# Kernel tuning notes

Measured on AMD Instinct MI355X. Metric: run time of the kernel, lower is better.

Reference implementation:

```python
import jax, jax.numpy as jnp
import numpy as np

B, S = 256, 64
D_SLOT, D_TEXT, H, E = 256, 768, 512, 512
VOCAB = 1000
D_IN = D_SLOT + D_TEXT


def setup_inputs() -> dict:
    key = jax.random.key(0)
    ks = jax.random.split(key, 12)
    w = 0.05  # small init so GRU gates are not saturated
    return {
        "slot_ids": jax.random.randint(ks[0], (B, S), 0, VOCAB),
        "value_embeds": jax.random.normal(ks[1], (B, S, D_TEXT), jnp.float32),
        "embed_table": jax.random.normal(ks[2], (VOCAB, D_SLOT), jnp.float32),
        "W_ih_f": jax.random.normal(ks[3], (3 * H, D_IN), jnp.float32) * w,
        "W_hh_f": jax.random.normal(ks[4], (3 * H, H), jnp.float32) * w,
        "b_ih_f": jax.random.normal(ks[5], (3 * H,), jnp.float32) * w,
        "b_hh_f": jax.random.normal(ks[6], (3 * H,), jnp.float32) * w,
        "W_ih_b": jax.random.normal(ks[7], (3 * H, D_IN), jnp.float32) * w,
        "W_hh_b": jax.random.normal(ks[8], (3 * H, H), jnp.float32) * w,
        "b_ih_b": jax.random.normal(ks[9], (3 * H,), jnp.float32) * w,
        "b_hh_b": jax.random.normal(ks[10], (3 * H,), jnp.float32) * w,
        "W_proj": jax.random.normal(ks[11], (E, 2 * H), jnp.float32) * w,
    }


def _gru(x, Wih, Whh, bih, bhh):
    # x: [S, B, D_IN] -> outputs [S, B, H]; PyTorch GRU cell math.
    h0 = jnp.zeros((x.shape[1], Whh.shape[1]), x.dtype)

    def step(h, xt):
        gi = xt @ Wih.T + bih          # [B, 3H]
        gh = h @ Whh.T + bhh           # [B, 3H]
        i_r, i_z, i_n = jnp.split(gi, 3, axis=-1)
        h_r, h_z, h_n = jnp.split(gh, 3, axis=-1)
        r = jax.nn.sigmoid(i_r + h_r)
        z = jax.nn.sigmoid(i_z + h_z)
        n = jnp.tanh(i_n + r * h_n)
        h_new = (1.0 - z) * n + z * h
        return h_new, h_new

    _, out = jax.lax.scan(step, h0, x)
    return out


def reference(slot_ids, value_embeds, embed_table, W_ih_f, W_hh_f, b_ih_f, b_hh_f,
              W_ih_b, W_hh_b, b_ih_b, b_hh_b, W_proj):
    # Per-frame: concat(slot embedding, value embedding) -> seq of slot-values.
    x = jnp.concatenate([embed_table[slot_ids], value_embeds], axis=-1)  # [B, S, D_IN]
    x = jnp.transpose(x, (1, 0, 2))                                      # [S, B, D_IN]
    out_f = _gru(x, W_ih_f, W_hh_f, b_ih_f, b_hh_f)                      # [S, B, H]
    out_b = _gru(x[::-1], W_ih_b, W_hh_b, b_ih_b, b_hh_b)[::-1]          # [S, B, H]
    out = jnp.concatenate([out_f, out_b], axis=-1)                       # [S, B, 2H]
    y = out @ W_proj.T                                                   # [S, B, E] (no bias)
    return jnp.transpose(y, (1, 0, 2))                                   # [B, S, E]
```

## Files before the change

### kernel.cpp

```cpp
#include <hip/hip_runtime.h>

typedef short v8s __attribute__((ext_vector_type(8)));
typedef float v4f __attribute__((ext_vector_type(4)));
typedef unsigned int v4u __attribute__((ext_vector_type(4)));
typedef unsigned long long u64;

static __device__ __forceinline__ unsigned short f2bf(float x) {
    unsigned u = __builtin_bit_cast(unsigned, x);
    unsigned r = (u + 0x7fffu + ((u >> 16) & 1u)) >> 16;
    return (unsigned short)r;
}

static __device__ __forceinline__ float sigm(float x) {
    return 1.f / (1.f + __expf(-x));
}
static __device__ __forceinline__ float tanh_fast(float x) {
    x = fminf(fmaxf(x, -15.f), 15.f);
    float e = __expf(2.f * x);
    return (e - 1.f) / (e + 1.f);
}

__global__ void cvt_bf16(const float* __restrict__ src, unsigned short* __restrict__ dst, int n) {
    int i = blockIdx.x * 256 + threadIdx.x;
    if (i < n) dst[i] = f2bf(src[i]);
}

__global__ void repack_whh(const float* __restrict__ src, unsigned short* __restrict__ dst) {
    long e = (long)blockIdx.x * 256 + threadIdx.x;
    int i = e & 7;
    int lane = (e >> 3) & 63;
    int kf = (e >> 9) & 15;
    int T = (int)(e >> 13);
    int gcol = T * 16 + (lane & 15);
    int k = kf * 32 + (lane >> 4) * 8 + i;
    dst[e] = f2bf(src[(long)gcol * 512 + k]);
}

__global__ void init_flags(unsigned int* __restrict__ p) {
    p[blockIdx.x * 256 + threadIdx.x] = 0;
}

__global__ void build_x(const int* __restrict__ slot_ids,
                        const float* __restrict__ value_embeds,
                        const float* __restrict__ embed_table,
                        unsigned short* __restrict__ X) {
    int r = blockIdx.x;
    int t = threadIdx.x;
    int id = slot_ids[r];
    X[(long)r * 1024 + t] = f2bf(embed_table[id * 256 + t]);
#pragma unroll
    for (int i = 0; i < 3; i++) {
        int c = t + i * 256;
        X[(long)r * 1024 + 256 + c] = f2bf(value_embeds[(long)r * 768 + c]);
    }
}

template <int EPI>
__global__ __launch_bounds__(256) void gemm_bt(const unsigned short* __restrict__ A,
                                               const unsigned short* __restrict__ Bt,
                                               float* __restrict__ C,
                                               int M, int N, int K) {
    const int LDT = 72;
    __shared__ unsigned short As[128 * 72];
    __shared__ unsigned short Bs[128 * 72];
    int tid = threadIdx.x;
    int lane = tid & 63;
    int wave = tid >> 6;
    int gm0 = blockIdx.y * 128;
    int gn0 = blockIdx.x * 128;
    int wm0 = (wave >> 1) * 64;
    int wn0 = (wave & 1) * 64;
    int q = lane >> 4;
    int l16 = lane & 15;

    v4f acc[4][4];
#pragma unroll
    for (int i = 0; i < 4; i++)
#pragma unroll
        for (int j = 0; j < 4; j++) acc[i][j] = v4f{0.f, 0.f, 0.f, 0.f};

    for (int k0 = 0; k0 < K; k0 += 64) {
#pragma unroll
        for (int l = tid; l < 1024; l += 256) {
            int row = l >> 3;
            int col = (l & 7) * 8;
            *(v8s*)&As[row * LDT + col] = *(const v8s*)&A[(long)(gm0 + row) * K + k0 + col];
            *(v8s*)&Bs[row * LDT + col] = *(const v8s*)&Bt[(long)(gn0 + row) * K + k0 + col];
        }
        __syncthreads();
#pragma unroll
        for (int kf = 0; kf < 2; kf++) {
            v8s af[4], bfr[4];
#pragma unroll
            for (int mi = 0; mi < 4; mi++)
                af[mi] = *(const v8s*)&As[(wm0 + mi * 16 + l16) * LDT + kf * 32 + q * 8];
#pragma unroll
            for (int ni = 0; ni < 4; ni++)
                bfr[ni] = *(const v8s*)&Bs[(wn0 + ni * 16 + l16) * LDT + kf * 32 + q * 8];
#pragma unroll
            for (int mi = 0; mi < 4; mi++)
#pragma unroll
                for (int ni = 0; ni < 4; ni++)
                    acc[mi][ni] = __builtin_amdgcn_mfma_f32_16x16x32_bf16(af[mi], bfr[ni], acc[mi][ni], 0, 0, 0);
        }
        __syncthreads();
    }

#pragma unroll
    for (int mi = 0; mi < 4; mi++)
#pragma unroll
        for (int ni = 0; ni < 4; ni++) {
            int col = gn0 + wn0 + ni * 16 + l16;
#pragma unroll
            for (int r = 0; r < 4; r++) {
                int row = gm0 + wm0 + mi * 16 + q * 4 + r;
                float v = acc[mi][ni][r];
                if (EPI == 0) {
                    C[(long)row * N + col] = v;
                } else {
                    int dd = (col >= 1536) ? 1 : 0;
                    int gcol = col - dd * 1536;
                    int g = gcol >> 9;
                    int jj = gcol & 511;
                    int cb = jj >> 5;
                    int jc = jj & 31;
                    int jhc = jc >> 4;
                    int l16c = jc & 15;
                    int b = row >> 6, s = row & 63;
                    int bg = b >> 5, brow = b & 31;
                    int rgc = brow >> 4, m = brow & 15;
                    int qc = m >> 2, rc = m & 3;
                    int wv = rgc * 2 + jhc;
                    long idx = (((((long)(dd * 64 + s) * 8 + bg) * 16 + cb) * 4 + wv) * 3 + g) * 256 +
                               (qc * 16 + l16c) * 4 + rc;
                    C[idx] = v;
                }
            }
        }
}

__global__ __launch_bounds__(256, 1) void gru_rec(const float* __restrict__ gi,
                                                  const unsigned short* __restrict__ Wpk,
                                                  const float* __restrict__ bih_f,
                                                  const float* __restrict__ bhh_f,
                                                  const float* __restrict__ bih_b,
                                                  const float* __restrict__ bhh_b,
                                                  unsigned short* __restrict__ hout,
                                                  unsigned int* __restrict__ hshd,
                                                  unsigned int* __restrict__ flags) {
    int tid = threadIdx.x;
    int lane = tid & 63;
    int wave = tid >> 6;
    int q = lane >> 4, l16 = lane & 15;
    int blk = blockIdx.x;
    int d = blk >> 7;
    int bg = (blk >> 4) & 7;
    int cb = blk & 15;
    int team = d * 8 + bg;
    int rg = wave >> 1, jh = wave & 1;
    int j = cb * 32 + jh * 16 + l16;

    v8s bfr[3][16];
#pragma unroll
    for (int g = 0; g < 3; g++) {
        const unsigned short* wp = Wpk + ((long)d * 96 + (g * 32 + cb * 2 + jh)) * 8192;
#pragma unroll
        for (int kf = 0; kf < 16; kf++)
            bfr[g][kf] = *(const v8s*)&wp[(kf * 64 + lane) * 8];
    }

    float bi[3], bh[3];
    {
        const float* bihp = d ? bih_b : bih_f;
        const float* bhhp = d ? bhh_b : bhh_f;
#pragma unroll
        for (int g = 0; g < 3; g++) {
            bi[g] = bihp[g * 512 + j];
            bh[g] = bhhp[g * 512 + j];
        }
    }
    float hreg[4] = {0.f, 0.f, 0.f, 0.f};

    unsigned int* myflags = flags + team * 64;
    unsigned int* hsteam = hshd + (long)team * 2 * 8192;

    v4f gir[3];
    {
        int s0 = d ? 63 : 0;
        const float* gp = gi + (((((long)(d * 64 + s0)) * 8 + bg) * 16 + cb) * 4 + wave) * 768 + lane * 4;
#pragma unroll
        for (int g = 0; g < 3; g++) gir[g] = __builtin_nontemporal_load((const v4f*)(gp + g * 256));
    }

    for (int t = 0; t < 64; t++) {
        int s = d ? (63 - t) : t;

        v4f acc[3];
#pragma unroll
        for (int g = 0; g < 3; g++) acc[g] = v4f{0.f, 0.f, 0.f, 0.f};

        if (t > 0) {
            while (__hip_atomic_load(&myflags[lane], __ATOMIC_RELAXED, __HIP_MEMORY_SCOPE_AGENT) <
                   (unsigned)t)
                __builtin_amdgcn_s_sleep(1);
            __builtin_amdgcn_sched_barrier(0);

            const char* hb = (const char*)hsteam + ((t + 1) & 1) * 32768 +
                             (rg * 16 + l16) * 1024 + q * 16;
            v4u a0, a1, a2, a3, a4, a5, a6, a7, a8, a9, a10, a11, a12, a13, a14, a15;
            asm volatile(
                "global_load_dwordx4 %0, %16, off sc1\n\t"
                "global_load_dwordx4 %1, %16, off offset:64 sc1\n\t"
                "global_load_dwordx4 %2, %16, off offset:128 sc1\n\t"
                "global_load_dwordx4 %3, %16, off offset:192 sc1\n\t"
                "global_load_dwordx4 %4, %16, off offset:256 sc1\n\t"
                "global_load_dwordx4 %5, %16, off offset:320 sc1\n\t"
                "global_load_dwordx4 %6, %16, off offset:384 sc1\n\t"
                "global_load_dwordx4 %7, %16, off offset:448 sc1\n\t"
                "global_load_dwordx4 %8, %16, off offset:512 sc1\n\t"
                "global_load_dwordx4 %9, %16, off offset:576 sc1\n\t"
                "global_load_dwordx4 %10, %16, off offset:640 sc1\n\t"
                "global_load_dwordx4 %11, %16, off offset:704 sc1\n\t"
                "global_load_dwordx4 %12, %16, off offset:768 sc1\n\t"
                "global_load_dwordx4 %13, %16, off offset:832 sc1\n\t"
                "global_load_dwordx4 %14, %16, off offset:896 sc1\n\t"
                "global_load_dwordx4 %15, %16, off offset:960 sc1"
                : "=&v"(a0), "=&v"(a1), "=&v"(a2), "=&v"(a3), "=&v"(a4), "=&v"(a5), "=&v"(a6),
                  "=&v"(a7), "=&v"(a8), "=&v"(a9), "=&v"(a10), "=&v"(a11), "=&v"(a12), "=&v"(a13),
                  "=&v"(a14), "=&v"(a15)
                : "v"(hb)
                : "memory");
            asm volatile("s_waitcnt vmcnt(0)" ::: "memory");
            __builtin_amdgcn_sched_barrier(0);

            v8s af[16];
            af[0] = __builtin_bit_cast(v8s, a0);
            af[1] = __builtin_bit_cast(v8s, a1);
            af[2] = __builtin_bit_cast(v8s, a2);
            af[3] = __builtin_bit_cast(v8s, a3);
            af[4] = __builtin_bit_cast(v8s, a4);
            af[5] = __builtin_bit_cast(v8s, a5);
            af[6] = __builtin_bit_cast(v8s, a6);
            af[7] = __builtin_bit_cast(v8s, a7);
            af[8] = __builtin_bit_cast(v8s, a8);
            af[9] = __builtin_bit_cast(v8s, a9);
            af[10] = __builtin_bit_cast(v8s, a10);
            af[11] = __builtin_bit_cast(v8s, a11);
            af[12] = __builtin_bit_cast(v8s, a12);
            af[13] = __builtin_bit_cast(v8s, a13);
            af[14] = __builtin_bit_cast(v8s, a14);
            af[15] = __builtin_bit_cast(v8s, a15);

#pragma unroll
            for (int kf = 0; kf < 16; kf++)
#pragma unroll
                for (int g = 0; g < 3; g++)
                    acc[g] = __builtin_amdgcn_mfma_f32_16x16x32_bf16(af[kf], bfr[g][kf], acc[g], 0, 0, 0);
        }

        unsigned int* dst = hsteam + (t & 1) * 8192;
        unsigned short hv[4];
#pragma unroll
        for (int r = 0; r < 4; r++) {
            float rr = sigm(gir[0][r] + bi[0] + acc[0][r] + bh[0]);
            float zz = sigm(gir[1][r] + bi[1] + acc[1][r] + bh[1]);
            float nn = tanh_fast(gir[2][r] + bi[2] + rr * (acc[2][r] + bh[2]));
            float hn = (1.f - zz) * nn + zz * hreg[r];
            hreg[r] = hn;
            hv[r] = f2bf(hn);
            float pv = __shfl_xor(hn, 1);
            if ((l16 & 1) == 0) {
                unsigned int pack = (unsigned int)hv[r] | ((unsigned int)f2bf(pv) << 16);
                int row = rg * 16 + q * 4 + r;
                __hip_atomic_store(&dst[row * 256 + (j >> 1)], pack, __ATOMIC_RELAXED,
                                   __HIP_MEMORY_SCOPE_AGENT);
            }
        }

        asm volatile("s_waitcnt vmcnt(0)" ::: "memory");
        if (lane == 0)
            __hip_atomic_store(&myflags[cb * 4 + wave], (unsigned)(t + 1), __ATOMIC_RELAXED,
                               __HIP_MEMORY_SCOPE_AGENT);

#pragma unroll
        for (int r = 0; r < 4; r++) {
            int row = rg * 16 + q * 4 + r;
            hout[((long)(bg * 32 + row) * 64 + s) * 1024 + d * 512 + j] = hv[r];
        }
        if (t < 63) {
            int sn = d ? (62 - t) : (t + 1);
            const float* gp =
                gi + (((((long)(d * 64 + sn)) * 8 + bg) * 16 + cb) * 4 + wave) * 768 + lane * 4;
#pragma unroll
            for (int g = 0; g < 3; g++) gir[g] = __builtin_nontemporal_load((const v4f*)(gp + g * 256));
        }
    }
}

extern "C" void kernel_launch(void* const* d_in, const int* in_sizes, int n_in,
                              void* d_out, int out_size, void* d_ws, size_t ws_size,
                              hipStream_t stream) {
    const int* slot_ids = (const int*)d_in[0];
    const float* value_embeds = (const float*)d_in[1];
    const float* embed_table = (const float*)d_in[2];
    const float* W_ih_f = (const float*)d_in[3];
    const float* W_hh_f = (const float*)d_in[4];
    const float* b_ih_f = (const float*)d_in[5];
    const float* b_hh_f = (const float*)d_in[6];
    const float* W_ih_b = (const float*)d_in[7];
    const float* W_hh_b = (const float*)d_in[8];
    const float* b_ih_b = (const float*)d_in[9];
    const float* b_hh_b = (const float*)d_in[10];
    const float* W_proj = (const float*)d_in[11];
    float* out = (float*)d_out;
    char* ws = (char*)d_ws;

    unsigned short* X = (unsigned short*)(ws + 0);
    float* gi = (float*)(ws + 33554432);
    unsigned short* Wstk = (unsigned short*)(ws + 234881024);
    unsigned short* Wpk = (unsigned short*)(ws + 241172480);
    unsigned short* Wp = (unsigned short*)(ws + 244318208);
    unsigned short* hout = X;
    unsigned int* hshd = (unsigned int*)Wstk;
    unsigned int* flags = (unsigned int*)(ws + 234881024 + 1048576);

    cvt_bf16<<<6144, 256, 0, stream>>>(W_ih_f, Wstk, 1536 * 1024);
    cvt_bf16<<<6144, 256, 0, stream>>>(W_ih_b, Wstk + 1536 * 1024, 1536 * 1024);
    repack_whh<<<3072, 256, 0, stream>>>(W_hh_f, Wpk);
    repack_whh<<<3072, 256, 0, stream>>>(W_hh_b, Wpk + 786432);
    cvt_bf16<<<2048, 256, 0, stream>>>(W_proj, Wp, 512 * 1024);
    build_x<<<16384, 256, 0, stream>>>(slot_ids, value_embeds, embed_table, X);

    gemm_bt<1><<<dim3(24, 128), 256, 0, stream>>>(X, Wstk, gi, 16384, 3072, 1024);

    init_flags<<<4, 256, 0, stream>>>(flags);

    gru_rec<<<256, 256, 0, stream>>>(gi, Wpk, b_ih_f, b_hh_f, b_ih_b, b_hh_b, hout, hshd, flags);

    gemm_bt<0><<<dim3(4, 128), 256, 0, stream>>>(hout, Wp, out, 16384, 512, 1024);
}
```

Before: 841.8 us.

## Stage GRU outputs in LDS and flush coalesced after recurrence; spin without sleep

Each GRU step now writes its packed bf16 hidden pairs into a 128KB shared-memory buffer instead of doing scattered 2-byte global stores to hout on the critical path. At the end the block copies the whole buffer out to hout with 16-byte vector stores. The flag spin loop also drops s_sleep, and an empty asm pins the W_hh fragments in registers. The trade-offs are a large LDS allocation, an extra serialized write phase at kernel end, and busier polling traffic on the flags.

```diff
diff --git a/kernel.cpp b/kernel.cpp
--- a/kernel.cpp
+++ b/kernel.cpp
@@ -139,6 +139,7 @@
         }
 }
 
+extern __shared__ __align__(16) char smem[];
 __global__ __launch_bounds__(256, 1) void gru_rec(const float* __restrict__ gi,
                                                   const unsigned short* __restrict__ Wpk,
                                                   const float* __restrict__ bih_f,
@@ -148,6 +149,7 @@
                                                   unsigned short* __restrict__ hout,
                                                   unsigned int* __restrict__ hshd,
                                                   unsigned int* __restrict__ flags) {
+    unsigned int* hl32 = (unsigned int*)smem;
     int tid = threadIdx.x;
     int lane = tid & 63;
     int wave = tid >> 6;
@@ -168,6 +170,11 @@
         for (int kf = 0; kf < 16; kf++)
             bfr[g][kf] = *(const v8s*)&wp[(kf * 64 + lane) * 8];
     }
+#pragma unroll
+    for (int g = 0; g < 3; g++)
+#pragma unroll
+        for (int kf = 0; kf < 16; kf++)
+            asm volatile("" : "+v"(bfr[g][kf]));
 
     float bi[3], bh[3];
     {
@@ -201,8 +208,8 @@
 
         if (t > 0) {
             while (__hip_atomic_load(&myflags[lane], __ATOMIC_RELAXED, __HIP_MEMORY_SCOPE_AGENT) <
-                   (unsigned)t)
-                __builtin_amdgcn_s_sleep(1);
+                   (unsigned)t) {
+            }
             __builtin_amdgcn_sched_barrier(0);
 
             const char* hb = (const char*)hsteam + ((t + 1) & 1) * 32768 +
@@ -259,21 +266,21 @@
         }
 
         unsigned int* dst = hsteam + (t & 1) * 8192;
-        unsigned short hv[4];
 #pragma unroll
         for (int r = 0; r < 4; r++) {
+            int row = rg * 16 + q * 4 + r;
             float rr = sigm(gir[0][r] + bi[0] + acc[0][r] + bh[0]);
             float zz = sigm(gir[1][r] + bi[1] + acc[1][r] + bh[1]);
             float nn = tanh_fast(gir[2][r] + bi[2] + rr * (acc[2][r] + bh[2]));
             float hn = (1.f - zz) * nn + zz * hreg[r];
             hreg[r] = hn;
-            hv[r] = f2bf(hn);
+            unsigned short hv = f2bf(hn);
             float pv = __shfl_xor(hn, 1);
             if ((l16 & 1) == 0) {
-                unsigned int pack = (unsigned int)hv[r] | ((unsigned int)f2bf(pv) << 16);
-                int row = rg * 16 + q * 4 + r;
+                unsigned int pack = (unsigned int)hv | ((unsigned int)f2bf(pv) << 16);
                 __hip_atomic_store(&dst[row * 256 + (j >> 1)], pack, __ATOMIC_RELAXED,
                                    __HIP_MEMORY_SCOPE_AGENT);
+                hl32[(row * 64 + s) * 16 + jh * 8 + (l16 >> 1)] = pack;
             }
         }
 
@@ -282,11 +289,6 @@
             __hip_atomic_store(&myflags[cb * 4 + wave], (unsigned)(t + 1), __ATOMIC_RELAXED,
                                __HIP_MEMORY_SCOPE_AGENT);
 
-#pragma unroll
-        for (int r = 0; r < 4; r++) {
-            int row = rg * 16 + q * 4 + r;
-            hout[((long)(bg * 32 + row) * 64 + s) * 1024 + d * 512 + j] = hv[r];
-        }
         if (t < 63) {
             int sn = d ? (62 - t) : (t + 1);
             const float* gp =
@@ -294,6 +296,15 @@
 #pragma unroll
             for (int g = 0; g < 3; g++) gir[g] = __builtin_nontemporal_load((const v4f*)(gp + g * 256));
         }
+    }
+
+    __syncthreads();
+    for (int u = tid; u < 8192; u += 256) {
+        int row = u >> 8;
+        int sx = (u >> 2) & 63;
+        int oc = u & 3;
+        v8s v = *(const v8s*)((const unsigned short*)smem + ((row * 64 + sx) * 32 + oc * 8));
+        *(v8s*)&hout[((long)(bg * 32 + row) * 64 + sx) * 1024 + d * 512 + cb * 32 + oc * 8] = v;
     }
 }
 
@@ -324,6 +335,9 @@
     unsigned int* hshd = (unsigned int*)Wstk;
     unsigned int* flags = (unsigned int*)(ws + 234881024 + 1048576);
 
+    const int SMEM = 131072;
+    hipFuncSetAttribute((const void*)gru_rec, hipFuncAttributeMaxDynamicSharedMemorySize, SMEM);
+
     cvt_bf16<<<6144, 256, 0, stream>>>(W_ih_f, Wstk, 1536 * 1024);
     cvt_bf16<<<6144, 256, 0, stream>>>(W_ih_b, Wstk + 1536 * 1024, 1536 * 1024);
     repack_whh<<<3072, 256, 0, stream>>>(W_hh_f, Wpk);
@@ -335,7 +349,7 @@
 
     init_flags<<<4, 256, 0, stream>>>(flags);
 
-    gru_rec<<<256, 256, 0, stream>>>(gi, Wpk, b_ih_f, b_hh_f, b_ih_b, b_hh_b, hout, hshd, flags);
+    gru_rec<<<256, 256, SMEM, stream>>>(gi, Wpk, b_ih_f, b_hh_f, b_ih_b, b_hh_b, hout, hshd, flags);
 
     gemm_bt<0><<<dim3(4, 128), 256, 0, stream>>>(hout, Wp, out, 16384, 512, 1024);
 }
```

Result: no change. 846.3 us (+0.5%).
